# Performance work log

Hardware: AMD Instinct MI355X
Metric: run time of the kernel (lower is better)

The kernel has to match this reference:

```python
import jax, jax.numpy as jnp
import numpy as np

N = 100000
E = 1600000
D = 256

def setup_inputs() -> dict:
    key = jax.random.key(0)
    k1, k2, k3 = jax.random.split(key, 3)
    nodes = jax.random.normal(k1, (N, D), dtype=jnp.float32)
    edge_index = jax.random.randint(k2, (2, E), 0, N, dtype=jnp.int64)
    W = jax.random.normal(k3, (D, D), dtype=jnp.float32) * 0.05  # GCN lin weight [out,in]
    b = jnp.zeros((D,), dtype=jnp.float32)
    gamma = jnp.ones((D,), dtype=jnp.float32)
    beta = jnp.zeros((D,), dtype=jnp.float32)
    return {"nodes": nodes, "edge_index": edge_index, "W": W, "b": b,
            "gamma": gamma, "beta": beta}

def reference(nodes, edge_index, W, b, gamma, beta):
    n = nodes.shape[0]
    loop = jnp.arange(n, dtype=edge_index.dtype)
    src = jnp.concatenate([edge_index[0], loop])  # add self-loops (PyG default)
    dst = jnp.concatenate([edge_index[1], loop])
    # linear transform
    x = nodes @ W.T  # [N, D]
    # symmetric normalization: deg from target index, weight 1 per edge
    deg = jnp.zeros((n,), dtype=x.dtype).at[dst].add(1.0)
    dinv = jnp.where(deg > 0, jax.lax.rsqrt(deg), 0.0)
    norm = dinv[src] * dinv[dst]  # [E+N]
    msg = x[src] * norm[:, None]
    out = jax.ops.segment_sum(msg, dst, num_segments=n) + b  # [N, D]
    # LayerNorm over feature dim
    mu = jnp.mean(out, axis=-1, keepdims=True)
    var = jnp.mean(jnp.square(out - mu), axis=-1, keepdims=True)
    out = (out - mu) * jax.lax.rsqrt(var + 1e-5) * gamma + beta
    # ReLU; dropout is identity in eval mode
    return jax.nn.relu(out)
```

## Files before the change

### kernel.cpp

```cpp
#include <hip/hip_runtime.h>
#include <hip/hip_bf16.h>

#define NN 100000
#define EE 1600000
#define DD 256
#define CAP 64
#define NPART 391
#define ABLK 512
#define ACHUNK 3125
#define SEGCAP 48

typedef __bf16 bf16x8 __attribute__((ext_vector_type(8)));
typedef float f32x4 __attribute__((ext_vector_type(4)));

__device__ __forceinline__ unsigned short f2bf(float f) {
    unsigned u = __builtin_bit_cast(unsigned, f);
    u += 0x7fffu + ((u >> 16) & 1u);
    return (unsigned short)(u >> 16);
}
__device__ __forceinline__ float bf2f(unsigned short h) {
    unsigned u = ((unsigned)h) << 16;
    return __builtin_bit_cast(float, u);
}

__global__ void k_detect(const unsigned long long* __restrict__ e64, int* __restrict__ flag) {
    if (threadIdx.x == 0 && blockIdx.x == 0) {
        int is32 = 0;
        for (int i = 0; i < 64; ++i)
            if (e64[i] > 0xFFFFFFFFULL) is32 = 1;
        *flag = is32;
    }
}

__global__ __launch_bounds__(256) void k_partA(const void* __restrict__ eptr,
        const int* __restrict__ flag, unsigned int* __restrict__ gseg,
        int* __restrict__ cnts) {
    __shared__ int lcnt[NPART];
    const int b = blockIdx.x, tid = threadIdx.x;
    for (int i = tid; i < NPART; i += 256) lcnt[i] = 0;
    __syncthreads();
    const int is32 = *flag;
    const int e0 = b * ACHUNK;
    for (int e = e0 + tid; e < e0 + ACHUNK; e += 256) {
        int s, d;
        if (is32) { const int* p = (const int*)eptr; s = p[e]; d = p[EE + e]; }
        else { const long long* p = (const long long*)eptr; s = (int)p[e]; d = (int)p[EE + e]; }
        const int pp = d >> 8, dl = d & 255;
        const int slot = atomicAdd(&lcnt[pp], 1);
        if (slot < SEGCAP)
            gseg[((size_t)pp * ABLK + b) * SEGCAP + slot] = ((unsigned)s << 8) | (unsigned)dl;
    }
    __syncthreads();
    for (int i = tid; i < NPART; i += 256)
        cnts[(size_t)i * ABLK + b] = min(lcnt[i], SEGCAP);
}

__global__ __launch_bounds__(256) void k_partB(const unsigned int* __restrict__ gseg,
        const int* __restrict__ cnts, int* __restrict__ bucket,
        int* __restrict__ cnt, float* __restrict__ dinv) {
    __shared__ int lc[256];
    __shared__ __align__(16) int lb[256 * CAP];
    const int p = blockIdx.x, tid = threadIdx.x;
    lc[tid] = 0;
    __syncthreads();
    #pragma unroll
    for (int half = 0; half < 2; ++half) {
        const int bb = half * 256 + tid;
        const int c = cnts[(size_t)p * ABLK + bb];
        const unsigned int* seg = gseg + ((size_t)p * ABLK + bb) * SEGCAP;
        for (int i = 0; i < c; ++i) {
            const unsigned int en = seg[i];
            const int d = en & 255;
            const int slot = atomicAdd(&lc[d], 1);
            if (slot < CAP) lb[d * CAP + slot] = (int)(en >> 8);
        }
    }
    __syncthreads();
    const size_t base = (size_t)p * 256 * CAP;
    #pragma unroll
    for (int it = 0; it < 16; ++it) {
        const int idx4 = it * 256 + tid;
        const int node = p * 256 + (idx4 >> 4);
        if (node < NN)
            *(uint4*)(bucket + base + (size_t)idx4 * 4) = *(const uint4*)&lb[idx4 * 4];
    }
    const int node = p * 256 + tid;
    if (node < NN) {
        const int c = lc[tid];
        cnt[node] = c;
        dinv[node] = rsqrtf((float)(c + 1));
    }
}

__global__ __launch_bounds__(256) void k_count_scatter(const void* __restrict__ eptr,
        const int* __restrict__ flag, int* __restrict__ cnt, int* __restrict__ bucket) {
    int e = blockIdx.x * 256 + threadIdx.x;
    if (e >= EE) return;
    int s, d;
    if (*flag) { const int* p = (const int*)eptr; s = p[e]; d = p[EE + e]; }
    else { const long long* p = (const long long*)eptr; s = (int)p[e]; d = (int)p[EE + e]; }
    int slot = atomicAdd(&cnt[d], 1);
    if (slot < CAP) bucket[d * CAP + slot] = s;
}

__global__ __launch_bounds__(256) void k_dinv(const int* __restrict__ cnt, float* __restrict__ dinv) {
    int v = blockIdx.x * 256 + threadIdx.x;
    if (v < NN) dinv[v] = rsqrtf((float)(cnt[v] + 1));
}

__global__ __launch_bounds__(256) void k_gemm(const float* __restrict__ nodes,
        const float* __restrict__ W, const float* __restrict__ dinv,
        unsigned short* __restrict__ y) {
    __shared__ __align__(16) unsigned short xlds[64][264];
    const int tid = threadIdx.x, lane = tid & 63, wv = tid >> 6;
    const int q = lane >> 4, n0 = lane & 15;

    bf16x8 afrag[8][4];
    #pragma unroll
    for (int g = 0; g < 4; ++g) {
        const int feat = wv * 64 + g * 16 + n0;
        const float* wp = W + (size_t)feat * 256 + q * 8;
        #pragma unroll
        for (int ks = 0; ks < 8; ++ks) {
            bf16x8 af;
            #pragma unroll
            for (int j = 0; j < 8; ++j)
                af[j] = __builtin_bit_cast(__bf16, f2bf(wp[ks * 32 + j]));
            afrag[ks][g] = af;
        }
    }

    const int row0 = blockIdx.x * 64;
    #pragma unroll
    for (int rr = 0; rr < 16; ++rr) {
        const int idx = rr * 256 + tid;
        const int r = idx >> 6, c4 = idx & 63;
        const int grow = min(row0 + r, NN - 1);
        const float4 v = *(const float4*)(nodes + (size_t)grow * 256 + c4 * 4);
        uint2 pk;
        pk.x = (unsigned)f2bf(v.x) | ((unsigned)f2bf(v.y) << 16);
        pk.y = (unsigned)f2bf(v.z) | ((unsigned)f2bf(v.w) << 16);
        *(uint2*)&xlds[r][c4 * 4] = pk;
    }
    __syncthreads();

    #pragma unroll
    for (int sub = 0; sub < 4; ++sub) {
        f32x4 acc[4] = {{0,0,0,0},{0,0,0,0},{0,0,0,0},{0,0,0,0}};
        #pragma unroll
        for (int ks = 0; ks < 8; ++ks) {
            const bf16x8 xf = *(const bf16x8*)&xlds[sub * 16 + n0][ks * 32 + q * 8];
            #pragma unroll
            for (int g = 0; g < 4; ++g)
                acc[g] = __builtin_amdgcn_mfma_f32_16x16x32_bf16(afrag[ks][g], xf, acc[g], 0, 0, 0);
        }
        const int node = row0 + sub * 16 + n0;
        if (node < NN) {
            const float dval = dinv[node];
            unsigned short* yp = y + (size_t)node * 256 + wv * 64 + q * 4;
            #pragma unroll
            for (int g = 0; g < 4; ++g) {
                uint2 pk;
                pk.x = (unsigned)f2bf(acc[g][0] * dval) | ((unsigned)f2bf(acc[g][1] * dval) << 16);
                pk.y = (unsigned)f2bf(acc[g][2] * dval) | ((unsigned)f2bf(acc[g][3] * dval) << 16);
                *(uint2*)(yp + g * 16) = pk;
            }
        }
    }
}

__global__ __launch_bounds__(256) void k_gather(const unsigned short* __restrict__ y,
        const int* __restrict__ cnt, const int* __restrict__ bucket,
        const float* __restrict__ dinv, const float* __restrict__ bias,
        const float* __restrict__ gamma, const float* __restrict__ beta,
        float* __restrict__ out) {
    const int v = blockIdx.x * 4 + (threadIdx.x >> 6);
    if (v >= NN) return;
    const int lane = threadIdx.x & 63;
    const int m = min(cnt[v], CAP);
    const int mysrc = (lane < m) ? bucket[v * CAP + lane] : 0;

    uint2 pk = *((const uint2*)(y + (size_t)v * 256) + lane);
    float a0 = bf2f((unsigned short)(pk.x & 0xffff));
    float a1 = bf2f((unsigned short)(pk.x >> 16));
    float a2 = bf2f((unsigned short)(pk.y & 0xffff));
    float a3 = bf2f((unsigned short)(pk.y >> 16));

    int j = 0;
    for (; j + 4 <= m; j += 4) {
        int s0 = __shfl(mysrc, j + 0);
        int s1 = __shfl(mysrc, j + 1);
        int s2 = __shfl(mysrc, j + 2);
        int s3 = __shfl(mysrc, j + 3);
        uint2 p0 = *((const uint2*)(y + (size_t)s0 * 256) + lane);
        uint2 p1 = *((const uint2*)(y + (size_t)s1 * 256) + lane);
        uint2 p2 = *((const uint2*)(y + (size_t)s2 * 256) + lane);
        uint2 p3 = *((const uint2*)(y + (size_t)s3 * 256) + lane);
        a0 += bf2f((unsigned short)(p0.x & 0xffff)) + bf2f((unsigned short)(p1.x & 0xffff))
            + bf2f((unsigned short)(p2.x & 0xffff)) + bf2f((unsigned short)(p3.x & 0xffff));
        a1 += bf2f((unsigned short)(p0.x >> 16)) + bf2f((unsigned short)(p1.x >> 16))
            + bf2f((unsigned short)(p2.x >> 16)) + bf2f((unsigned short)(p3.x >> 16));
        a2 += bf2f((unsigned short)(p0.y & 0xffff)) + bf2f((unsigned short)(p1.y & 0xffff))
            + bf2f((unsigned short)(p2.y & 0xffff)) + bf2f((unsigned short)(p3.y & 0xffff));
        a3 += bf2f((unsigned short)(p0.y >> 16)) + bf2f((unsigned short)(p1.y >> 16))
            + bf2f((unsigned short)(p2.y >> 16)) + bf2f((unsigned short)(p3.y >> 16));
    }
    for (; j < m; ++j) {
        int s = __shfl(mysrc, j);
        uint2 p = *((const uint2*)(y + (size_t)s * 256) + lane);
        a0 += bf2f((unsigned short)(p.x & 0xffff));
        a1 += bf2f((unsigned short)(p.x >> 16));
        a2 += bf2f((unsigned short)(p.y & 0xffff));
        a3 += bf2f((unsigned short)(p.y >> 16));
    }

    const float dvv = dinv[v];
    const float4 bb = *(const float4*)(bias + lane * 4);
    float u0 = a0 * dvv + bb.x;
    float u1 = a1 * dvv + bb.y;
    float u2 = a2 * dvv + bb.z;
    float u3 = a3 * dvv + bb.w;

    float s1 = u0 + u1 + u2 + u3;
    float s2 = u0 * u0 + u1 * u1 + u2 * u2 + u3 * u3;
    #pragma unroll
    for (int o = 32; o > 0; o >>= 1) {
        s1 += __shfl_xor(s1, o);
        s2 += __shfl_xor(s2, o);
    }
    const float mean = s1 * (1.0f / 256.0f);
    const float var  = s2 * (1.0f / 256.0f) - mean * mean;
    const float rstd = rsqrtf(var + 1e-5f);

    const float4 g  = *(const float4*)(gamma + lane * 4);
    const float4 be = *(const float4*)(beta + lane * 4);
    float4 o4;
    o4.x = fmaxf(0.0f, (u0 - mean) * rstd * g.x + be.x);
    o4.y = fmaxf(0.0f, (u1 - mean) * rstd * g.y + be.y);
    o4.z = fmaxf(0.0f, (u2 - mean) * rstd * g.z + be.z);
    o4.w = fmaxf(0.0f, (u3 - mean) * rstd * g.w + be.w);
    *(float4*)(out + (size_t)v * 256 + lane * 4) = o4;
}

extern "C" void kernel_launch(void* const* d_in, const int* in_sizes, int n_in,
                              void* d_out, int out_size, void* d_ws, size_t ws_size,
                              hipStream_t stream) {
    const float* nodes = (const float*)d_in[0];
    const void*  edges = d_in[1];
    const float* W     = (const float*)d_in[2];
    const float* b     = (const float*)d_in[3];
    const float* gamma = (const float*)d_in[4];
    const float* beta  = (const float*)d_in[5];
    float* out = (float*)d_out;

    char* ws = (char*)d_ws;
    size_t off = 0;
    auto alloc = [&](size_t bytes) { size_t p = off; off = (off + bytes + 255) & ~(size_t)255; return p; };
    int*            cnt    = (int*)(ws + alloc((size_t)NN * 4));
    float*          dinv   = (float*)(ws + alloc((size_t)NN * 4));
    int*            flag   = (int*)(ws + alloc(256));
    int*            bucket = (int*)(ws + alloc((size_t)NN * CAP * 4));
    unsigned short* y      = (unsigned short*)(ws + alloc((size_t)NN * DD * 2));
    const size_t base_need = off;
    int*            cnts   = (int*)(ws + alloc((size_t)NPART * ABLK * 4));
    unsigned int*   gseg   = (unsigned int*)(ws + alloc((size_t)NPART * ABLK * SEGCAP * 4));
    const size_t full_need = off;
    (void)in_sizes; (void)n_in; (void)out_size; (void)base_need;

    k_detect<<<1, 64, 0, stream>>>((const unsigned long long*)edges, flag);
    if (ws_size >= full_need) {
        k_partA<<<ABLK, 256, 0, stream>>>(edges, flag, gseg, cnts);
        k_partB<<<NPART, 256, 0, stream>>>(gseg, cnts, bucket, cnt, dinv);
    } else {
        hipMemsetAsync(cnt, 0, (size_t)NN * 4, stream);
        k_count_scatter<<<(EE + 255) / 256, 256, 0, stream>>>(edges, flag, cnt, bucket);
        k_dinv<<<(NN + 255) / 256, 256, 0, stream>>>(cnt, dinv);
    }
    k_gemm<<<(NN + 63) / 64, 256, 0, stream>>>(nodes, W, dinv, y);
    k_gather<<<NN / 4, 256, 0, stream>>>(y, cnt, bucket, dinv, b, gamma, beta, out);
}
```

Measured before the change: 415.6 us.

## Exact-size edge partitioning, pre-swizzled bf16 weights, self-loop in bucket, 16B gathers

Partition pass A now counts edges per partition first, prefix-sums the counts, and writes compact exactly-sized segments, which removes the SEGCAP=48 truncation. The edge-width detection moves into each partA block. A small kernel converts W to bf16 once in MFMA fragment order, so each GEMM block loads fragments directly instead of converting fp32 weights. The self-loop is stored as the first bucket entry with count starting at 1, and dinv is recomputed from cnt instead of being stored. The gather has each half-wave fetch a different neighbor with 16-byte loads, doubling per-lane load width, at the cost of a cross-half reduction and a second pass over edges in partA.

```diff
diff --git a/kernel.cpp b/kernel.cpp
--- a/kernel.cpp
+++ b/kernel.cpp
@@ -8,7 +8,6 @@
 #define NPART 391
 #define ABLK 512
 #define ACHUNK 3125
-#define SEGCAP 48
 
 typedef __bf16 bf16x8 __attribute__((ext_vector_type(8)));
 typedef float f32x4 __attribute__((ext_vector_type(4)));
@@ -21,6 +20,90 @@
 __device__ __forceinline__ float bf2f(unsigned short h) {
     unsigned u = ((unsigned)h) << 16;
     return __builtin_bit_cast(float, u);
+}
+
+__global__ __launch_bounds__(256) void k_partA(const void* __restrict__ eptr,
+        unsigned int* __restrict__ gseg2, int* __restrict__ cnts, int* __restrict__ pref) {
+    __shared__ int lcnt[NPART];
+    __shared__ int lcnt2[NPART];
+    __shared__ int lpref[NPART];
+    __shared__ int sA[512], sB[512];
+    __shared__ int lflag;
+    const int b = blockIdx.x, tid = threadIdx.x;
+    if (tid == 0) lflag = 0;
+    for (int i = tid; i < NPART; i += 256) { lcnt[i] = 0; lcnt2[i] = 0; }
+    __syncthreads();
+    if (tid < 64) {
+        const unsigned long long w = ((const unsigned long long*)eptr)[tid];
+        if (w > 0xFFFFFFFFULL) lflag = 1;
+    }
+    __syncthreads();
+    const int is32 = lflag;
+    const int e0 = b * ACHUNK;
+    for (int e = e0 + tid; e < e0 + ACHUNK; e += 256) {
+        const int d = is32 ? ((const int*)eptr)[EE + e]
+                           : (int)((const long long*)eptr)[EE + e];
+        atomicAdd(&lcnt[d >> 8], 1);
+    }
+    __syncthreads();
+    sA[tid]       = (tid < NPART) ? lcnt[tid] : 0;
+    sA[tid + 256] = (tid + 256 < NPART) ? lcnt[tid + 256] : 0;
+    __syncthreads();
+    int* s = sA; int* d2 = sB;
+    for (int off = 1; off < 512; off <<= 1) {
+        d2[tid]       = s[tid]       + (tid >= off ? s[tid - off] : 0);
+        d2[tid + 256] = s[tid + 256] + (tid + 256 >= off ? s[tid + 256 - off] : 0);
+        __syncthreads();
+        int* t = s; s = d2; d2 = t;
+    }
+    for (int i = tid; i < NPART; i += 256) {
+        lpref[i] = (i == 0) ? 0 : s[i - 1];
+        cnts[(size_t)i * ABLK + b] = lcnt[i];
+        pref[(size_t)i * ABLK + b] = (i == 0) ? 0 : s[i - 1];
+    }
+    __syncthreads();
+    for (int e = e0 + tid; e < e0 + ACHUNK; e += 256) {
+        int ss, dd;
+        if (is32) { const int* p = (const int*)eptr; ss = p[e]; dd = p[EE + e]; }
+        else { const long long* p = (const long long*)eptr; ss = (int)p[e]; dd = (int)p[EE + e]; }
+        const int pp = dd >> 8;
+        const int slot = atomicAdd(&lcnt2[pp], 1);
+        gseg2[(size_t)b * ACHUNK + lpref[pp] + slot] = ((unsigned)ss << 8) | (unsigned)(dd & 255);
+    }
+}
+
+__global__ __launch_bounds__(256) void k_partB(const unsigned int* __restrict__ gseg2,
+        const int* __restrict__ cnts, const int* __restrict__ pref,
+        int* __restrict__ bucket, int* __restrict__ cnt) {
+    __shared__ int lc[256];
+    __shared__ __align__(16) int lb[256 * CAP];
+    const int p = blockIdx.x, tid = threadIdx.x;
+    const int node0 = p * 256 + tid;
+    lc[tid] = 1;
+    lb[tid * CAP] = node0;
+    __syncthreads();
+    #pragma unroll
+    for (int half = 0; half < 2; ++half) {
+        const int bb = half * 256 + tid;
+        const int c = cnts[(size_t)p * ABLK + bb];
+        const unsigned int* seg = gseg2 + (size_t)bb * ACHUNK + pref[(size_t)p * ABLK + bb];
+        for (int i = 0; i < c; ++i) {
+            const unsigned int en = seg[i];
+            const int d = en & 255;
+            const int slot = atomicAdd(&lc[d], 1);
+            if (slot < CAP) lb[d * CAP + slot] = (int)(en >> 8);
+        }
+    }
+    __syncthreads();
+    const size_t base = (size_t)p * 256 * CAP;
+    #pragma unroll
+    for (int it = 0; it < 16; ++it) {
+        const int idx4 = it * 256 + tid;
+        const int node = p * 256 + (idx4 >> 4);
+        if (node < NN)
+            *(uint4*)(bucket + base + (size_t)idx4 * 4) = *(const uint4*)&lb[idx4 * 4];
+    }
+    if (node0 < NN) cnt[node0] = lc[tid];
 }
 
 __global__ void k_detect(const unsigned long long* __restrict__ e64, int* __restrict__ flag) {
@@ -31,67 +114,10 @@
         *flag = is32;
     }
 }
-
-__global__ __launch_bounds__(256) void k_partA(const void* __restrict__ eptr,
-        const int* __restrict__ flag, unsigned int* __restrict__ gseg,
-        int* __restrict__ cnts) {
-    __shared__ int lcnt[NPART];
-    const int b = blockIdx.x, tid = threadIdx.x;
-    for (int i = tid; i < NPART; i += 256) lcnt[i] = 0;
-    __syncthreads();
-    const int is32 = *flag;
-    const int e0 = b * ACHUNK;
-    for (int e = e0 + tid; e < e0 + ACHUNK; e += 256) {
-        int s, d;
-        if (is32) { const int* p = (const int*)eptr; s = p[e]; d = p[EE + e]; }
-        else { const long long* p = (const long long*)eptr; s = (int)p[e]; d = (int)p[EE + e]; }
-        const int pp = d >> 8, dl = d & 255;
-        const int slot = atomicAdd(&lcnt[pp], 1);
-        if (slot < SEGCAP)
-            gseg[((size_t)pp * ABLK + b) * SEGCAP + slot] = ((unsigned)s << 8) | (unsigned)dl;
-    }
-    __syncthreads();
-    for (int i = tid; i < NPART; i += 256)
-        cnts[(size_t)i * ABLK + b] = min(lcnt[i], SEGCAP);
-}
-
-__global__ __launch_bounds__(256) void k_partB(const unsigned int* __restrict__ gseg,
-        const int* __restrict__ cnts, int* __restrict__ bucket,
-        int* __restrict__ cnt, float* __restrict__ dinv) {
-    __shared__ int lc[256];
-    __shared__ __align__(16) int lb[256 * CAP];
-    const int p = blockIdx.x, tid = threadIdx.x;
-    lc[tid] = 0;
-    __syncthreads();
-    #pragma unroll
-    for (int half = 0; half < 2; ++half) {
-        const int bb = half * 256 + tid;
-        const int c = cnts[(size_t)p * ABLK + bb];
-        const unsigned int* seg = gseg + ((size_t)p * ABLK + bb) * SEGCAP;
-        for (int i = 0; i < c; ++i) {
-            const unsigned int en = seg[i];
-            const int d = en & 255;
-            const int slot = atomicAdd(&lc[d], 1);
-            if (slot < CAP) lb[d * CAP + slot] = (int)(en >> 8);
-        }
-    }
-    __syncthreads();
-    const size_t base = (size_t)p * 256 * CAP;
-    #pragma unroll
-    for (int it = 0; it < 16; ++it) {
-        const int idx4 = it * 256 + tid;
-        const int node = p * 256 + (idx4 >> 4);
-        if (node < NN)
-            *(uint4*)(bucket + base + (size_t)idx4 * 4) = *(const uint4*)&lb[idx4 * 4];
-    }
-    const int node = p * 256 + tid;
-    if (node < NN) {
-        const int c = lc[tid];
-        cnt[node] = c;
-        dinv[node] = rsqrtf((float)(c + 1));
-    }
-}
-
+__global__ __launch_bounds__(256) void k_init(int* __restrict__ cnt, int* __restrict__ bucket) {
+    int v = blockIdx.x * 256 + threadIdx.x;
+    if (v < NN) { cnt[v] = 1; bucket[(size_t)v * CAP] = v; }
+}
 __global__ __launch_bounds__(256) void k_count_scatter(const void* __restrict__ eptr,
         const int* __restrict__ flag, int* __restrict__ cnt, int* __restrict__ bucket) {
     int e = blockIdx.x * 256 + threadIdx.x;
@@ -100,16 +126,30 @@
     if (*flag) { const int* p = (const int*)eptr; s = p[e]; d = p[EE + e]; }
     else { const long long* p = (const long long*)eptr; s = (int)p[e]; d = (int)p[EE + e]; }
     int slot = atomicAdd(&cnt[d], 1);
-    if (slot < CAP) bucket[d * CAP + slot] = s;
-}
-
-__global__ __launch_bounds__(256) void k_dinv(const int* __restrict__ cnt, float* __restrict__ dinv) {
-    int v = blockIdx.x * 256 + threadIdx.x;
-    if (v < NN) dinv[v] = rsqrtf((float)(cnt[v] + 1));
+    if (slot < CAP) bucket[(size_t)d * CAP + slot] = s;
+}
+
+__global__ __launch_bounds__(256) void k_wconv(const float* __restrict__ W,
+        unsigned short* __restrict__ wf) {
+    const int s = blockIdx.x * 256 + threadIdx.x;
+    const int lane = s & 63;
+    const int ks = (s >> 6) & 7;
+    const int g  = (s >> 9) & 3;
+    const int wv = s >> 11;
+    const int feat = wv * 64 + g * 16 + (lane & 15);
+    const int k0 = ks * 32 + (lane >> 4) * 8;
+    const float* wp = W + (size_t)feat * 256 + k0;
+    unsigned short o[8];
+    #pragma unroll
+    for (int j = 0; j < 8; ++j) o[j] = f2bf(wp[j]);
+    uint4 pk;
+    pk.x = o[0] | ((unsigned)o[1] << 16); pk.y = o[2] | ((unsigned)o[3] << 16);
+    pk.z = o[4] | ((unsigned)o[5] << 16); pk.w = o[6] | ((unsigned)o[7] << 16);
+    *(uint4*)(wf + (size_t)s * 8) = pk;
 }
 
 __global__ __launch_bounds__(256) void k_gemm(const float* __restrict__ nodes,
-        const float* __restrict__ W, const float* __restrict__ dinv,
+        const unsigned short* __restrict__ wf, const int* __restrict__ cnt,
         unsigned short* __restrict__ y) {
     __shared__ __align__(16) unsigned short xlds[64][264];
     const int tid = threadIdx.x, lane = tid & 63, wv = tid >> 6;
@@ -117,18 +157,10 @@
 
     bf16x8 afrag[8][4];
     #pragma unroll
-    for (int g = 0; g < 4; ++g) {
-        const int feat = wv * 64 + g * 16 + n0;
-        const float* wp = W + (size_t)feat * 256 + q * 8;
+    for (int g = 0; g < 4; ++g)
         #pragma unroll
-        for (int ks = 0; ks < 8; ++ks) {
-            bf16x8 af;
-            #pragma unroll
-            for (int j = 0; j < 8; ++j)
-                af[j] = __builtin_bit_cast(__bf16, f2bf(wp[ks * 32 + j]));
-            afrag[ks][g] = af;
-        }
-    }
+        for (int ks = 0; ks < 8; ++ks)
+            afrag[ks][g] = *(const bf16x8*)(wf + ((((size_t)wv * 4 + g) * 8 + ks) * 64 + lane) * 8);
 
     const int row0 = blockIdx.x * 64;
     #pragma unroll
@@ -156,7 +188,7 @@
         }
         const int node = row0 + sub * 16 + n0;
         if (node < NN) {
-            const float dval = dinv[node];
+            const float dval = rsqrtf((float)cnt[node]);
             unsigned short* yp = y + (size_t)node * 256 + wv * 64 + q * 4;
             #pragma unroll
             for (int g = 0; g < 4; ++g) {
@@ -171,60 +203,77 @@
 
 __global__ __launch_bounds__(256) void k_gather(const unsigned short* __restrict__ y,
         const int* __restrict__ cnt, const int* __restrict__ bucket,
-        const float* __restrict__ dinv, const float* __restrict__ bias,
-        const float* __restrict__ gamma, const float* __restrict__ beta,
-        float* __restrict__ out) {
+        const float* __restrict__ bias, const float* __restrict__ gamma,
+        const float* __restrict__ beta, float* __restrict__ out) {
     const int v = blockIdx.x * 4 + (threadIdx.x >> 6);
-    if (v >= NN) return;
     const int lane = threadIdx.x & 63;
-    const int m = min(cnt[v], CAP);
-    const int mysrc = (lane < m) ? bucket[v * CAP + lane] : 0;
-
-    uint2 pk = *((const uint2*)(y + (size_t)v * 256) + lane);
-    float a0 = bf2f((unsigned short)(pk.x & 0xffff));
-    float a1 = bf2f((unsigned short)(pk.x >> 16));
-    float a2 = bf2f((unsigned short)(pk.y & 0xffff));
-    float a3 = bf2f((unsigned short)(pk.y >> 16));
+    const int h = lane >> 5, l = lane & 31;
+    const int c = cnt[v];
+    const int m = min(c, CAP);
+    const int my = (lane < m) ? bucket[(size_t)v * CAP + lane] : 0;
+
+    float acc[8] = {0, 0, 0, 0, 0, 0, 0, 0};
+    #define ACCUM(P) do {                                                   \
+        acc[0] += bf2f((unsigned short)((P).x & 0xffff));                   \
+        acc[1] += bf2f((unsigned short)((P).x >> 16));                      \
+        acc[2] += bf2f((unsigned short)((P).y & 0xffff));                   \
+        acc[3] += bf2f((unsigned short)((P).y >> 16));                      \
+        acc[4] += bf2f((unsigned short)((P).z & 0xffff));                   \
+        acc[5] += bf2f((unsigned short)((P).z >> 16));                      \
+        acc[6] += bf2f((unsigned short)((P).w & 0xffff));                   \
+        acc[7] += bf2f((unsigned short)((P).w >> 16));                      \
+    } while (0)
 
     int j = 0;
+    for (; j + 8 <= m; j += 8) {
+        const int s0 = __shfl(my, j + h);
+        const int s1 = __shfl(my, j + 2 + h);
+        const int s2 = __shfl(my, j + 4 + h);
+        const int s3 = __shfl(my, j + 6 + h);
+        const uint4 p0 = *((const uint4*)(y + (size_t)s0 * 256) + l);
+        const uint4 p1 = *((const uint4*)(y + (size_t)s1 * 256) + l);
+        const uint4 p2 = *((const uint4*)(y + (size_t)s2 * 256) + l);
+        const uint4 p3 = *((const uint4*)(y + (size_t)s3 * 256) + l);
+        ACCUM(p0); ACCUM(p1); ACCUM(p2); ACCUM(p3);
+    }
     for (; j + 4 <= m; j += 4) {
-        int s0 = __shfl(mysrc, j + 0);
-        int s1 = __shfl(mysrc, j + 1);
-        int s2 = __shfl(mysrc, j + 2);
-        int s3 = __shfl(mysrc, j + 3);
-        uint2 p0 = *((const uint2*)(y + (size_t)s0 * 256) + lane);
-        uint2 p1 = *((const uint2*)(y + (size_t)s1 * 256) + lane);
-        uint2 p2 = *((const uint2*)(y + (size_t)s2 * 256) + lane);
-        uint2 p3 = *((const uint2*)(y + (size_t)s3 * 256) + lane);
-        a0 += bf2f((unsigned short)(p0.x & 0xffff)) + bf2f((unsigned short)(p1.x & 0xffff))
-            + bf2f((unsigned short)(p2.x & 0xffff)) + bf2f((unsigned short)(p3.x & 0xffff));
-        a1 += bf2f((unsigned short)(p0.x >> 16)) + bf2f((unsigned short)(p1.x >> 16))
-            + bf2f((unsigned short)(p2.x >> 16)) + bf2f((unsigned short)(p3.x >> 16));
-        a2 += bf2f((unsigned short)(p0.y & 0xffff)) + bf2f((unsigned short)(p1.y & 0xffff))
-            + bf2f((unsigned short)(p2.y & 0xffff)) + bf2f((unsigned short)(p3.y & 0xffff));
-        a3 += bf2f((unsigned short)(p0.y >> 16)) + bf2f((unsigned short)(p1.y >> 16))
-            + bf2f((unsigned short)(p2.y >> 16)) + bf2f((unsigned short)(p3.y >> 16));
-    }
-    for (; j < m; ++j) {
-        int s = __shfl(mysrc, j);
-        uint2 p = *((const uint2*)(y + (size_t)s * 256) + lane);
-        a0 += bf2f((unsigned short)(p.x & 0xffff));
-        a1 += bf2f((unsigned short)(p.x >> 16));
-        a2 += bf2f((unsigned short)(p.y & 0xffff));
-        a3 += bf2f((unsigned short)(p.y >> 16));
-    }
-
-    const float dvv = dinv[v];
-    const float4 bb = *(const float4*)(bias + lane * 4);
-    float u0 = a0 * dvv + bb.x;
-    float u1 = a1 * dvv + bb.y;
-    float u2 = a2 * dvv + bb.z;
-    float u3 = a3 * dvv + bb.w;
-
-    float s1 = u0 + u1 + u2 + u3;
-    float s2 = u0 * u0 + u1 * u1 + u2 * u2 + u3 * u3;
-    #pragma unroll
-    for (int o = 32; o > 0; o >>= 1) {
+        const int s0 = __shfl(my, j + h);
+        const int s1 = __shfl(my, j + 2 + h);
+        const uint4 p0 = *((const uint4*)(y + (size_t)s0 * 256) + l);
+        const uint4 p1 = *((const uint4*)(y + (size_t)s1 * 256) + l);
+        ACCUM(p0); ACCUM(p1);
+    }
+    for (; j + 2 <= m; j += 2) {
+        const int s0 = __shfl(my, j + h);
+        const uint4 p0 = *((const uint4*)(y + (size_t)s0 * 256) + l);
+        ACCUM(p0);
+    }
+    if (j < m) {
+        const int st = __shfl(my, j);
+        if (h == 0) {
+            const uint4 p0 = *((const uint4*)(y + (size_t)st * 256) + l);
+            ACCUM(p0);
+        }
+    }
+    #undef ACCUM
+
+    #pragma unroll
+    for (int i = 0; i < 8; ++i) acc[i] += __shfl_xor(acc[i], 32);
+
+    const float dvv = rsqrtf((float)c);
+    const float4 b0 = *(const float4*)(bias + l * 8);
+    const float4 b1 = *(const float4*)(bias + l * 8 + 4);
+    float u[8];
+    u[0] = acc[0] * dvv + b0.x; u[1] = acc[1] * dvv + b0.y;
+    u[2] = acc[2] * dvv + b0.z; u[3] = acc[3] * dvv + b0.w;
+    u[4] = acc[4] * dvv + b1.x; u[5] = acc[5] * dvv + b1.y;
+    u[6] = acc[6] * dvv + b1.z; u[7] = acc[7] * dvv + b1.w;
+
+    float s1 = 0, s2 = 0;
+    #pragma unroll
+    for (int i = 0; i < 8; ++i) { s1 += u[i]; s2 += u[i] * u[i]; }
+    #pragma unroll
+    for (int o = 16; o > 0; o >>= 1) {
         s1 += __shfl_xor(s1, o);
         s2 += __shfl_xor(s2, o);
     }
@@ -232,14 +281,23 @@
     const float var  = s2 * (1.0f / 256.0f) - mean * mean;
     const float rstd = rsqrtf(var + 1e-5f);
 
-    const float4 g  = *(const float4*)(gamma + lane * 4);
-    const float4 be = *(const float4*)(beta + lane * 4);
-    float4 o4;
-    o4.x = fmaxf(0.0f, (u0 - mean) * rstd * g.x + be.x);
-    o4.y = fmaxf(0.0f, (u1 - mean) * rstd * g.y + be.y);
-    o4.z = fmaxf(0.0f, (u2 - mean) * rstd * g.z + be.z);
-    o4.w = fmaxf(0.0f, (u3 - mean) * rstd * g.w + be.w);
-    *(float4*)(out + (size_t)v * 256 + lane * 4) = o4;
+    const float4 g0 = *(const float4*)(gamma + l * 8);
+    const float4 g1 = *(const float4*)(gamma + l * 8 + 4);
+    const float4 e0 = *(const float4*)(beta + l * 8);
+    const float4 e1 = *(const float4*)(beta + l * 8 + 4);
+    float o8[8];
+    o8[0] = fmaxf(0.0f, (u[0] - mean) * rstd * g0.x + e0.x);
+    o8[1] = fmaxf(0.0f, (u[1] - mean) * rstd * g0.y + e0.y);
+    o8[2] = fmaxf(0.0f, (u[2] - mean) * rstd * g0.z + e0.z);
+    o8[3] = fmaxf(0.0f, (u[3] - mean) * rstd * g0.w + e0.w);
+    o8[4] = fmaxf(0.0f, (u[4] - mean) * rstd * g1.x + e1.x);
+    o8[5] = fmaxf(0.0f, (u[5] - mean) * rstd * g1.y + e1.y);
+    o8[6] = fmaxf(0.0f, (u[6] - mean) * rstd * g1.z + e1.z);
+    o8[7] = fmaxf(0.0f, (u[7] - mean) * rstd * g1.w + e1.w);
+    float4 ov;
+    if (h == 0) { ov.x = o8[0]; ov.y = o8[1]; ov.z = o8[2]; ov.w = o8[3]; }
+    else        { ov.x = o8[4]; ov.y = o8[5]; ov.z = o8[6]; ov.w = o8[7]; }
+    *(float4*)(out + (size_t)v * 256 + l * 8 + h * 4) = ov;
 }
 
 extern "C" void kernel_launch(void* const* d_in, const int* in_sizes, int n_in,
@@ -257,25 +315,25 @@
     size_t off = 0;
     auto alloc = [&](size_t bytes) { size_t p = off; off = (off + bytes + 255) & ~(size_t)255; return p; };
     int*            cnt    = (int*)(ws + alloc((size_t)NN * 4));
-    float*          dinv   = (float*)(ws + alloc((size_t)NN * 4));
     int*            flag   = (int*)(ws + alloc(256));
     int*            bucket = (int*)(ws + alloc((size_t)NN * CAP * 4));
     unsigned short* y      = (unsigned short*)(ws + alloc((size_t)NN * DD * 2));
-    const size_t base_need = off;
+    unsigned short* wf     = (unsigned short*)(ws + alloc((size_t)DD * DD * 2));
     int*            cnts   = (int*)(ws + alloc((size_t)NPART * ABLK * 4));
-    unsigned int*   gseg   = (unsigned int*)(ws + alloc((size_t)NPART * ABLK * SEGCAP * 4));
+    int*            pref   = (int*)(ws + alloc((size_t)NPART * ABLK * 4));
+    unsigned int*   gseg2  = (unsigned int*)(ws + alloc((size_t)EE * 4));
     const size_t full_need = off;
-    (void)in_sizes; (void)n_in; (void)out_size; (void)base_need;
-
-    k_detect<<<1, 64, 0, stream>>>((const unsigned long long*)edges, flag);
+    (void)in_sizes; (void)n_in; (void)out_size;
+
+    k_wconv<<<32, 256, 0, stream>>>(W, wf);
     if (ws_size >= full_need) {
-        k_partA<<<ABLK, 256, 0, stream>>>(edges, flag, gseg, cnts);
-        k_partB<<<NPART, 256, 0, stream>>>(gseg, cnts, bucket, cnt, dinv);
+        k_partA<<<ABLK, 256, 0, stream>>>(edges, gseg2, cnts, pref);
+        k_partB<<<NPART, 256, 0, stream>>>(gseg2, cnts, pref, bucket, cnt);
     } else {
-        hipMemsetAsync(cnt, 0, (size_t)NN * 4, stream);
+        k_detect<<<1, 64, 0, stream>>>((const unsigned long long*)edges, flag);
+        k_init<<<(NN + 255) / 256, 256, 0, stream>>>(cnt, bucket);
         k_count_scatter<<<(EE + 255) / 256, 256, 0, stream>>>(edges, flag, cnt, bucket);
-        k_dinv<<<(NN + 255) / 256, 256, 0, stream>>>(cnt, dinv);
-    }
-    k_gemm<<<(NN + 63) / 64, 256, 0, stream>>>(nodes, W, dinv, y);
-    k_gather<<<NN / 4, 256, 0, stream>>>(y, cnt, bucket, dinv, b, gamma, beta, out);
-}
+    }
+    k_gemm<<<(NN + 63) / 64, 256, 0, stream>>>(nodes, wf, cnt, y);
+    k_gather<<<NN / 4, 256, 0, stream>>>(y, cnt, bucket, b, gamma, beta, out);
+}
```

Result: faster. 374.5 us (-9.9%).
